# Kernel tuning notes

Measured on AMD Instinct MI355X. Metric: run time of the kernel, lower is better.

The kernel has to match this reference:

```python
import jax, jax.numpy as jnp
import numpy as np

NUM_CLASSES = 16384
FEATURE_DIM = 128
LAMBDA_PARAM = 0.005
EPS = 1e-12  # matches torch F.normalize clamp_min eps


def setup_inputs() -> dict:
    key = jax.random.key(0)
    k1, k2 = jax.random.split(key)
    z = jax.random.normal(k1, (NUM_CLASSES, FEATURE_DIM), dtype=jnp.float32)
    labels = jax.random.randint(k2, (NUM_CLASSES,), 0, NUM_CLASSES, dtype=jnp.int32)
    return {"z": z, "labels": labels}


def _l2_normalize(x):
    # torch F.normalize(dim=1): x / max(||x||, eps); zero rows stay zero.
    n = jnp.linalg.norm(x, axis=1, keepdims=True)
    return x / jnp.maximum(n, EPS)


def reference(z, labels):
    # per-class mean via single segment reduce (replaces the per-class python loop)
    counts = jax.ops.segment_sum(jnp.ones_like(labels, dtype=z.dtype), labels,
                                 num_segments=NUM_CLASSES)            # [C]
    sums = jax.ops.segment_sum(z, labels, num_segments=NUM_CLASSES)   # [C, D]
    has = counts > 0
    centers = jnp.where(has[:, None], sums / jnp.maximum(counts, 1.0)[:, None], 0.0)

    z_norm = _l2_normalize(z)                 # [B, D]
    centers_norm = _l2_normalize(centers)     # [C, D]
    batch_size = z.shape[0]
    c = (z_norm @ centers_norm.T) / batch_size  # [B, C], square since B == C

    diag = jnp.diagonal(c)
    invariance_loss = jnp.sum((diag - 1.0) ** 2)
    redundancy_reduction_loss = jnp.sum(c ** 2) - jnp.sum(diag ** 2)  # off-diagonal sq sum
    return invariance_loss + LAMBDA_PARAM * redundancy_reduction_loss
```

## Files before the change

kernel.cpp:

```cpp
#include <hip/hip_runtime.h>
#include <hip/hip_fp16.h>

#define NC 16384
#define FD 128
#define LAMBDA 0.005f
#define SLOTCAP 64
#define NPAIR 128

typedef __attribute__((ext_vector_type(8))) short short8;
typedef __attribute__((ext_vector_type(4))) float f32x4;

__device__ __forceinline__ float wave_sum(float v) {
#pragma unroll
  for (int m = 32; m > 0; m >>= 1) v += __shfl_xor(v, m, 64);
  return v;
}

__device__ __forceinline__ unsigned pack_bf16(float x, float y) {
  unsigned ux = __float_as_uint(x), uy = __float_as_uint(y);
  ux = (ux + 0x7FFFu + ((ux >> 16) & 1u)) >> 16;
  uy = (uy + 0x7FFFu + ((uy >> 16) & 1u)) >> 16;
  return ux | (uy << 16);
}

__global__ __launch_bounds__(256) void zero_kernel(int4* __restrict__ cnt4,
                                                   float* __restrict__ scal) {
  cnt4[blockIdx.x * 256 + threadIdx.x] = make_int4(0, 0, 0, 0);
  if (blockIdx.x == 0 && threadIdx.x < 16) scal[threadIdx.x] = 0.f;
}

__global__ __launch_bounds__(256) void scatter_kernel(
    const int* __restrict__ labels, int* __restrict__ cnt, int* __restrict__ slot) {
  int i = blockIdx.x * 256 + threadIdx.x;
  int lab = labels[i];
  int p = atomicAdd(&cnt[lab], 1);
  if (p < SLOTCAP) slot[(size_t)lab * SLOTCAP + p] = i;
}

__global__ __launch_bounds__(256) void center_kernel(
    const float* __restrict__ z, const int* __restrict__ cnt,
    const int* __restrict__ slot, unsigned* __restrict__ cnb,
    unsigned* __restrict__ znb, float2* __restrict__ dpart) {
  __shared__ float red[8];
  int t = threadIdx.x, wave = t >> 6, lane = t & 63;
  int c = blockIdx.x * 4 + wave;

  int4 s4 = *(const int4*)&slot[(size_t)c * SLOTCAP];
  int n = cnt[c];
  float2 a = *(const float2*)&z[(size_t)c * FD + lane * 2];
  if (n > SLOTCAP) n = SLOTCAP;

  int i0 = n > 0 ? s4.x : c, i1 = n > 1 ? s4.y : c;
  int i2 = n > 2 ? s4.z : c, i3 = n > 3 ? s4.w : c;
  float2 v0 = *(const float2*)&z[(size_t)i0 * FD + lane * 2];
  float2 v1 = *(const float2*)&z[(size_t)i1 * FD + lane * 2];
  float2 v2 = *(const float2*)&z[(size_t)i2 * FD + lane * 2];
  float2 v3 = *(const float2*)&z[(size_t)i3 * FD + lane * 2];
  float2 s = make_float2(0.f, 0.f);
  if (n > 0) { s.x += v0.x; s.y += v0.y; }
  if (n > 1) { s.x += v1.x; s.y += v1.y; }
  if (n > 2) { s.x += v2.x; s.y += v2.y; }
  if (n > 3) { s.x += v3.x; s.y += v3.y; }
  for (int k = 4; k < n; ++k) {
    int i = slot[(size_t)c * SLOTCAP + k];
    float2 v = *(const float2*)&z[(size_t)i * FD + lane * 2];
    s.x += v.x; s.y += v.y;
  }
  float inv = n > 0 ? 1.0f / (float)n : 0.0f;
  s.x *= inv; s.y *= inv;
  float sc = wave_sum(s.x * s.x + s.y * s.y);
  float ic = 1.0f / fmaxf(sqrtf(sc), 1e-12f);
  s.x *= ic; s.y *= ic;
  cnb[(size_t)c * 64 + lane] = pack_bf16(s.x, s.y);

  float na = wave_sum(a.x * a.x + a.y * a.y);
  float ia = 1.0f / fmaxf(sqrtf(na), 1e-12f);
  float dd = wave_sum(a.x * s.x + a.y * s.y);
  float d = dd * ia;
  znb[(size_t)c * 64 + lane] = pack_bf16(a.x * ia, a.y * ia);

  if (lane == 0) { red[wave * 2] = d; red[wave * 2 + 1] = d * d; }
  __syncthreads();
  if (t == 0) {
    dpart[blockIdx.x] = make_float2(red[0] + red[2] + red[4] + red[6],
                                    red[1] + red[3] + red[5] + red[7]);
  }
}

__global__ __launch_bounds__(256) void gram_kernel(
    const unsigned short* __restrict__ znb, const unsigned short* __restrict__ cnb,
    __half2* __restrict__ pz, __half2* __restrict__ pc) {
  __shared__ char lds[33280];
  unsigned short* Bu = (unsigned short*)lds;
  int t = threadIdx.x, wave = t >> 6, lane = t & 63;
  int b = blockIdx.x, m = b & 1, pair = b >> 1;
  const unsigned short* Ab = m ? cnb : znb;

  {
    const int4* src = (const int4*)(Ab + (size_t)pair * 16384);
#pragma unroll
    for (int k = 0; k < 8; ++k) {
      int idx = k * 256 + t;
      int q = idx >> 10, idx2 = idx & 1023;
      int row = idx2 >> 4, col8 = idx2 & 15;
      *(int4*)&Bu[q * 8320 + row * 130 + col8 * 8] = src[idx];
    }
  }
  __syncthreads();

  f32x4 acc[2][8];
#pragma unroll
  for (int i = 0; i < 2; ++i)
#pragma unroll
    for (int j = 0; j < 8; ++j)
      acc[i][j] = (f32x4){0.f, 0.f, 0.f, 0.f};

#pragma unroll
  for (int q = 0; q < 2; ++q) {
    const unsigned short* Bl = Bu + q * 8320 + (lane >> 4) * (8 * 130) + (lane & 15);
    short8 fr[2][8];
#pragma unroll
    for (int kb = 0; kb < 2; ++kb)
#pragma unroll
      for (int cb = 0; cb < 8; ++cb)
#pragma unroll
        for (int j = 0; j < 8; ++j)
          fr[kb][cb][j] = (short)Bl[kb * 4160 + cb * 16 + j * 130];
    short8 fa[2][2];
#pragma unroll
    for (int til = 0; til < 2; ++til)
#pragma unroll
      for (int kb = 0; kb < 2; ++kb)
#pragma unroll
        for (int j = 0; j < 8; ++j)
          fa[til][kb][j] = (short)Bl[kb * 4160 + (wave * 2 + til) * 16 + j * 130];
#pragma unroll
    for (int til = 0; til < 2; ++til)
#pragma unroll
      for (int tj = 0; tj < 8; ++tj) {
        acc[til][tj] = __builtin_amdgcn_mfma_f32_16x16x32_bf16(
            fa[til][0], fr[0][tj], acc[til][tj], 0, 0, 0);
        acc[til][tj] = __builtin_amdgcn_mfma_f32_16x16x32_bf16(
            fa[til][1], fr[1][tj], acc[til][tj], 0, 0, 0);
      }
  }
  __syncthreads();

  unsigned short* G = (unsigned short*)lds;
#pragma unroll
  for (int til = 0; til < 2; ++til)
#pragma unroll
    for (int tj = 0; tj < 8; ++tj)
#pragma unroll
      for (int q = 0; q < 4; ++q) {
        int d = (wave * 2 + til) * 16 + (lane >> 4) * 4 + q;
        int e = tj * 16 + (lane & 15);
        __half h = __float2half(acc[til][tj][q]);
        G[d * 130 + e] = *(unsigned short*)&h;
      }
  __syncthreads();

  unsigned* Pg = (unsigned*)((m ? pc : pz) + (size_t)pair * 8192);
#pragma unroll
  for (int it = 0; it < 32; ++it) {
    int row = it * 4 + (t >> 6);
    int h2i = t & 63;
    Pg[row * 64 + h2i] = *(const unsigned*)(lds + row * 260 + h2i * 4);
  }
}

__global__ __launch_bounds__(256) void reduce_final_kernel(
    const __half2* __restrict__ pz, const __half2* __restrict__ pc,
    const float2* __restrict__ dpart, float* __restrict__ scal,
    int* __restrict__ ticket_p, float* __restrict__ out) {
  __shared__ float2 lz[4][64], lc[4][64];
  __shared__ float rr[2][4];
  __shared__ int tk;
  int t = threadIdx.x, wave = t >> 6, lane = t & 63;
  int e2 = blockIdx.x * 64 + lane;
  float2 sz = make_float2(0.f, 0.f), sc = make_float2(0.f, 0.f);
  for (int k = 0; k < NPAIR / 4; ++k) {
    size_t c = (size_t)(wave * (NPAIR / 4) + k) * 8192 + e2;
    float2 fz = __half22float2(pz[c]);
    float2 fc = __half22float2(pc[c]);
    sz.x += fz.x; sz.y += fz.y;
    sc.x += fc.x; sc.y += fc.y;
  }
  lz[wave][lane] = sz;
  lc[wave][lane] = sc;
  __syncthreads();
  if (wave == 0) {
    float2 tz = make_float2(0.f, 0.f), tc = make_float2(0.f, 0.f);
#pragma unroll
    for (int w = 0; w < 4; ++w) {
      tz.x += lz[w][lane].x; tz.y += lz[w][lane].y;
      tc.x += lc[w][lane].x; tc.y += lc[w][lane].y;
    }
    float S = wave_sum(tz.x * tc.x + tz.y * tc.y);
    if (lane == 0) {
      unsafeAtomicAdd(&scal[2], S);
      __threadfence();
      tk = atomicAdd(ticket_p, 1);
    }
  }
  __syncthreads();
  if (tk == 127) {
    float a1 = 0.f, a2 = 0.f;
#pragma unroll
    for (int k = 0; k < 16; ++k) {
      float2 d = dpart[k * 256 + t];
      a1 += d.x; a2 += d.y;
    }
    a1 = wave_sum(a1);
    a2 = wave_sum(a2);
    if (lane == 0) { rr[0][wave] = a1; rr[1][wave] = a2; }
    __syncthreads();
    if (t == 0) {
      float SS = atomicAdd(&scal[2], 0.0f);
      double S1 = (double)rr[0][0] + rr[0][1] + rr[0][2] + rr[0][3];
      double S2 = (double)rr[1][0] + rr[1][1] + rr[1][2] + rr[1][3];
      double Sall = SS;
      double B = (double)NC;
      double inv_loss = S2 / (B * B) - 2.0 * S1 / B + (double)NC;
      double red_loss = (Sall - S2) / (B * B);
      out[0] = (float)(inv_loss + (double)LAMBDA * red_loss);
    }
  }
}

extern "C" void kernel_launch(void* const* d_in, const int* in_sizes, int n_in,
                              void* d_out, int out_size, void* d_ws, size_t ws_size,
                              hipStream_t stream) {
  const float* z = (const float*)d_in[0];
  const int* labels = (const int*)d_in[1];
  float* out = (float*)d_out;
  float* ws = (float*)d_ws;

  __half2* pz = (__half2*)ws;
  __half2* pc = pz + (size_t)NPAIR * 8192;
  unsigned* znb = (unsigned*)(pc + (size_t)NPAIR * 8192);
  unsigned* cnb = znb + (size_t)NC * 64;
  float2* dpart = (float2*)(cnb + (size_t)NC * 64);
  float* scal = (float*)(dpart + 4096);
  int* cnt = (int*)(scal + 16);
  int* slot = cnt + NC;
  int* ticket = (int*)&scal[8];

  zero_kernel<<<NC / 1024, 256, 0, stream>>>((int4*)cnt, scal);
  scatter_kernel<<<NC / 256, 256, 0, stream>>>(labels, cnt, slot);
  center_kernel<<<NC / 4, 256, 0, stream>>>(z, cnt, slot, cnb, znb, dpart);
  gram_kernel<<<2 * NPAIR, 256, 0, stream>>>((const unsigned short*)znb,
                                             (const unsigned short*)cnb, pz, pc);
  reduce_final_kernel<<<128, 256, 0, stream>>>(pz, pc, dpart, scal, ticket, out);
}
```

Measured before the change: 37.67 us.

## Fuse gram and final reduce kernels via atomic ticket and spin-wait barrier

```diff
diff --git a/kernel.cpp b/kernel.cpp
--- a/kernel.cpp
+++ b/kernel.cpp
@@ -6,6 +6,8 @@
 #define LAMBDA 0.005f
 #define SLOTCAP 64
 #define NPAIR 128
+#define NGB (2 * NPAIR)
+#define NRB 128
 
 typedef __attribute__((ext_vector_type(8))) short short8;
 typedef __attribute__((ext_vector_type(4))) float f32x4;
@@ -87,9 +89,11 @@
   }
 }
 
-__global__ __launch_bounds__(256) void gram_kernel(
+__global__ __launch_bounds__(256) void gram_reduce_kernel(
     const unsigned short* __restrict__ znb, const unsigned short* __restrict__ cnb,
-    __half2* __restrict__ pz, __half2* __restrict__ pc) {
+    __half2* __restrict__ pz, __half2* __restrict__ pc,
+    const float2* __restrict__ dpart, float* __restrict__ scal,
+    int* __restrict__ ticket_p, int* __restrict__ qc, float* __restrict__ out) {
   __shared__ char lds[33280];
   unsigned short* Bu = (unsigned short*)lds;
   int t = threadIdx.x, wave = t >> 6, lane = t & 63;
@@ -167,17 +171,28 @@
     int h2i = t & 63;
     Pg[row * 64 + h2i] = *(const unsigned*)(lds + row * 260 + h2i * 4);
   }
-}
-
-__global__ __launch_bounds__(256) void reduce_final_kernel(
-    const __half2* __restrict__ pz, const __half2* __restrict__ pc,
-    const float2* __restrict__ dpart, float* __restrict__ scal,
-    int* __restrict__ ticket_p, float* __restrict__ out) {
-  __shared__ float2 lz[4][64], lc[4][64];
-  __shared__ float rr[2][4];
-  __shared__ int tk;
-  int t = threadIdx.x, wave = t >> 6, lane = t & 63;
-  int e2 = blockIdx.x * 64 + lane;
+
+  __shared__ int stk;
+  if (t == 0) {
+    __threadfence();
+    stk = atomicAdd(qc, 1);
+  }
+  __syncthreads();
+  int tk0 = stk;
+  if (tk0 < NGB - NRB) return;
+  if (t == 0) {
+    while (__hip_atomic_load(qc, __ATOMIC_ACQUIRE, __HIP_MEMORY_SCOPE_AGENT) < NGB)
+      __builtin_amdgcn_s_sleep(16);
+    __threadfence();
+  }
+  __syncthreads();
+  int rblk = tk0 - (NGB - NRB);
+
+  float2* lz = (float2*)lds;
+  float2* lc = lz + 256;
+  float* rr = (float*)(lc + 256);
+  int* tkp = (int*)(rr + 8);
+  int e2 = rblk * 64 + lane;
   float2 sz = make_float2(0.f, 0.f), sc = make_float2(0.f, 0.f);
   for (int k = 0; k < NPAIR / 4; ++k) {
     size_t c = (size_t)(wave * (NPAIR / 4) + k) * 8192 + e2;
@@ -186,25 +201,25 @@
     sz.x += fz.x; sz.y += fz.y;
     sc.x += fc.x; sc.y += fc.y;
   }
-  lz[wave][lane] = sz;
-  lc[wave][lane] = sc;
+  lz[wave * 64 + lane] = sz;
+  lc[wave * 64 + lane] = sc;
   __syncthreads();
   if (wave == 0) {
     float2 tz = make_float2(0.f, 0.f), tc = make_float2(0.f, 0.f);
 #pragma unroll
     for (int w = 0; w < 4; ++w) {
-      tz.x += lz[w][lane].x; tz.y += lz[w][lane].y;
-      tc.x += lc[w][lane].x; tc.y += lc[w][lane].y;
+      tz.x += lz[w * 64 + lane].x; tz.y += lz[w * 64 + lane].y;
+      tc.x += lc[w * 64 + lane].x; tc.y += lc[w * 64 + lane].y;
     }
     float S = wave_sum(tz.x * tc.x + tz.y * tc.y);
     if (lane == 0) {
       unsafeAtomicAdd(&scal[2], S);
       __threadfence();
-      tk = atomicAdd(ticket_p, 1);
-    }
-  }
-  __syncthreads();
-  if (tk == 127) {
+      tkp[0] = atomicAdd(ticket_p, 1);
+    }
+  }
+  __syncthreads();
+  if (tkp[0] == NRB - 1) {
     float a1 = 0.f, a2 = 0.f;
 #pragma unroll
     for (int k = 0; k < 16; ++k) {
@@ -213,12 +228,12 @@
     }
     a1 = wave_sum(a1);
     a2 = wave_sum(a2);
-    if (lane == 0) { rr[0][wave] = a1; rr[1][wave] = a2; }
+    if (lane == 0) { rr[wave] = a1; rr[4 + wave] = a2; }
     __syncthreads();
     if (t == 0) {
       float SS = atomicAdd(&scal[2], 0.0f);
-      double S1 = (double)rr[0][0] + rr[0][1] + rr[0][2] + rr[0][3];
-      double S2 = (double)rr[1][0] + rr[1][1] + rr[1][2] + rr[1][3];
+      double S1 = (double)rr[0] + rr[1] + rr[2] + rr[3];
+      double S2 = (double)rr[4] + rr[5] + rr[6] + rr[7];
       double Sall = SS;
       double B = (double)NC;
       double inv_loss = S2 / (B * B) - 2.0 * S1 / B + (double)NC;
@@ -245,11 +260,12 @@
   int* cnt = (int*)(scal + 16);
   int* slot = cnt + NC;
   int* ticket = (int*)&scal[8];
+  int* qc = (int*)&scal[12];
 
   zero_kernel<<<NC / 1024, 256, 0, stream>>>((int4*)cnt, scal);
   scatter_kernel<<<NC / 256, 256, 0, stream>>>(labels, cnt, slot);
   center_kernel<<<NC / 4, 256, 0, stream>>>(z, cnt, slot, cnb, znb, dpart);
-  gram_kernel<<<2 * NPAIR, 256, 0, stream>>>((const unsigned short*)znb,
-                                             (const unsigned short*)cnb, pz, pc);
-  reduce_final_kernel<<<128, 256, 0, stream>>>(pz, pc, dpart, scal, ticket, out);
-}
+  gram_reduce_kernel<<<NGB, 256, 0, stream>>>((const unsigned short*)znb,
+                                              (const unsigned short*)cnb, pz, pc,
+                                              dpart, scal, ticket, qc, out);
+}
```

New measurement: 51.03 us. +35.4%, slower.
